# Performance work log

Hardware: AMD Instinct MI355X
Metric: run time of the kernel (lower is better)

The kernel has to match this reference:

```python
import jax, jax.numpy as jnp
import numpy as np

B = 262144
HIST = 24
FORE = 20
HID = 256
# torch: tau_int = clamp(tau,1,18).long().item(); default tau=6.0 -> static 6 (host sync in torch)
TAU_INT = 6


def setup_inputs() -> dict:
    key = jax.random.key(0)
    ks = jax.random.split(key, 9)
    s = 0.1
    return {
        "history": jax.random.normal(ks[0], (B, HIST), jnp.float32),
        "enc_w1": jax.random.normal(ks[1], (HIST + FORE, HID), jnp.float32) * s,
        "enc_b1": jnp.zeros((HID,), jnp.float32),
        "enc_w2": jax.random.normal(ks[2], (HID, HID), jnp.float32) * s,
        "enc_b2": jnp.zeros((HID,), jnp.float32),
        "cor_w1": jax.random.normal(ks[3], (HID, HID), jnp.float32) * s,
        "cor_b1": jnp.zeros((HID,), jnp.float32),
        "cor_w2": jax.random.normal(ks[4], (HID, FORE), jnp.float32) * s,
        "cor_b2": jnp.zeros((FORE,), jnp.float32),
        "alpha": jnp.float32(0.2),
        "beta": jnp.float32(0.3),
        "gamma": jnp.float32(0.01),
        "tau": jnp.float32(6.0),
        "lambda_mix": jnp.float32(0.5),
    }


def _physics_core(history, alpha, beta, gamma, steps):
    a = jax.nn.sigmoid(alpha)
    b = jax.nn.sigmoid(beta)
    g = jnp.abs(gamma)
    T0 = history[:, -1]                      # [B]
    buf0 = history[:, -TAU_INT:].T           # [tau, B]; buf0[0] = history[:, -tau]

    def step(carry, _):
        T, buf = carry
        T_delayed = buf[0]
        T_new = T - a * T - b * T_delayed - g * T ** 3
        buf = jnp.concatenate([buf[1:], T_new[None, :]], axis=0)
        return (T_new, buf), T_new

    _, preds = jax.lax.scan(step, (T0, buf0), None, length=steps)
    return preds.T                            # [B, steps]


def reference(history, enc_w1, enc_b1, enc_w2, enc_b2,
              cor_w1, cor_b1, cor_w2, cor_b2,
              alpha, beta, gamma, tau, lambda_mix):
    T_physics = _physics_core(history, alpha, beta, gamma, FORE)   # [B, FORE]
    combined = jnp.concatenate([history, T_physics], axis=1)       # [B, HIST+FORE]
    h = jnp.tanh(combined @ enc_w1 + enc_b1)
    features = jnp.tanh(h @ enc_w2 + enc_b2)
    c = jnp.tanh(features @ cor_w1 + cor_b1)
    T_soft = c @ cor_w2 + cor_b2                                   # [B, FORE]
    lam = jax.nn.sigmoid(lambda_mix)
    T_pred = T_physics + lam * T_soft
    return (T_pred, T_physics, T_soft)
```

## Files before the change

kernel.cpp:

```cpp
#include <hip/hip_runtime.h>
#include <hip/hip_bf16.h>

#define NROWS 262144
#define HISTC 24
#define FOREC 20

typedef __bf16        v8bf __attribute__((ext_vector_type(8)));
typedef float         v4f  __attribute__((ext_vector_type(4)));
typedef float         v2f  __attribute__((ext_vector_type(2)));
typedef unsigned int  v4u  __attribute__((ext_vector_type(4)));
typedef unsigned int  v2u  __attribute__((ext_vector_type(2)));

#define WS_WT1_OFF 64
#define WT1_ELEMS 16384
#define WT2_ELEMS 65536
#define WT3_ELEMS 65536
#define WT4R_ELEMS 65536

#define TANH_C 2.885390081777927f

__device__ __forceinline__ unsigned short f2bf(float x) {
    unsigned u = __builtin_bit_cast(unsigned, x);
    u += 0x7FFFu + ((u >> 16) & 1u);
    return (unsigned short)(u >> 16);
}

__device__ __forceinline__ unsigned packbf2(float a, float b) {
    unsigned ua = __builtin_bit_cast(unsigned, a) + 0x8000u;
    unsigned ub = __builtin_bit_cast(unsigned, b) + 0x8000u;
    return __builtin_amdgcn_perm(ub, ua, 0x07060302u);
}

__device__ __forceinline__ void lds_barrier() {
    asm volatile("s_waitcnt lgkmcnt(0)\n\ts_barrier" ::: "memory");
}

__global__ __launch_bounds__(256) void prep_kernel(
        const float* __restrict__ w1, const float* __restrict__ w2,
        const float* __restrict__ w3, const float* __restrict__ w4,
        const float* __restrict__ alpha, const float* __restrict__ beta,
        const float* __restrict__ gamma, const float* __restrict__ lmix,
        unsigned char* __restrict__ ws)
{
    __shared__ unsigned short tile[4][32 * 17];
    if (blockIdx.x == 104) {
        int t = threadIdx.x;
        float* wsf = (float*)ws;
        if (t == 0) wsf[0] = 1.0f / (1.0f + expf(-alpha[0]));
        else if (t == 1) wsf[1] = 1.0f / (1.0f + expf(-beta[0]));
        else if (t == 2) wsf[2] = fabsf(gamma[0]);
        else if (t == 3) wsf[3] = 1.0f / (1.0f + expf(-lmix[0]));
        return;
    }
    const int w    = threadIdx.x >> 6;
    const int lane = threadIdx.x & 63;
    const int g    = blockIdx.x * 4 + w;
    const float* src; int srcN, Kreal, Nreal, nt, kt;
    if (g < 32)       { src = w1; srcN = 256; Kreal = 44;  Nreal = 256; nt = g >> 1;  kt = g & 1; }
    else if (g < 160) { int t = g - 32;  src = w2; srcN = 256; Kreal = 256; Nreal = 256; nt = t >> 3; kt = t & 7; }
    else if (g < 288) { int t = g - 160; src = w3; srcN = 256; Kreal = 256; Nreal = 256; nt = t >> 3; kt = t & 7; }
    else              { int t = g - 288; src = w4; srcN = 20;  Kreal = 256; Nreal = 20;  nt = (t >> 3) & 1; kt = t & 7; }

    const int kbase = kt * 32;
    const int fl = lane & 15;
    const int rl = lane >> 4;
    const int feat = nt * 16 + fl;
    unsigned short* tl = tile[w];

#pragma unroll
    for (int it = 0; it < 8; ++it) {
        int row = it * 4 + rl;
        int k = kbase + row;
        float v = (k < Kreal && feat < Nreal) ? src[k * srcN + feat] : 0.0f;
        tl[row * 17 + fl] = f2bf(v);
    }
    __syncthreads();

    const int qq = lane >> 4;
    unsigned short e0 = tl[(qq * 8 + 0) * 17 + fl];
    unsigned short e1 = tl[(qq * 8 + 1) * 17 + fl];
    unsigned short e2 = tl[(qq * 8 + 2) * 17 + fl];
    unsigned short e3 = tl[(qq * 8 + 3) * 17 + fl];
    unsigned short e4 = tl[(qq * 8 + 4) * 17 + fl];
    unsigned short e5 = tl[(qq * 8 + 5) * 17 + fl];
    unsigned short e6 = tl[(qq * 8 + 6) * 17 + fl];
    unsigned short e7 = tl[(qq * 8 + 7) * 17 + fl];
    v4u pk;
    pk[0] = e0 | ((unsigned)e1 << 16);
    pk[1] = e2 | ((unsigned)e3 << 16);
    pk[2] = e4 | ((unsigned)e5 << 16);
    pk[3] = e6 | ((unsigned)e7 << 16);
    unsigned short* dst = (unsigned short*)(ws + WS_WT1_OFF);
    *(v4u*)&dst[(g * 64 + lane) * 8] = pk;
}

template<int KT, int KTN>
__device__ __forceinline__ void layer_pipe(unsigned short* buf,
        const v4u* __restrict__ wp, const v4u* __restrict__ wpn,
        const float* __restrict__ bias, v4u A[2][4],
        int w, int c, int q, int lane)
{
    v4f acc[4][4];
#pragma unroll
    for (int ft = 0; ft < 4; ++ft)
#pragma unroll
        for (int st = 0; st < 4; ++st) {
            v4f z = {0.0f, 0.0f, 0.0f, 0.0f};
            acc[ft][st] = z;
        }

#pragma unroll
    for (int kt = 0; kt < KT; ++kt) {
        const int cs = kt & 1;
        const int ps = cs ^ 1;
        if (kt + 1 < KT) {
#pragma unroll
            for (int ft = 0; ft < 4; ++ft)
                A[ps][ft] = wp[((w * 4 + ft) * KT + kt + 1) * 64 + lane];
        } else {
#pragma unroll
            for (int ft = 0; ft < 4; ++ft)
                A[ps][ft] = wpn[((w * 4 + ft) * KTN + 0) * 64 + lane];
        }
#pragma unroll
        for (int st = 0; st < 4; ++st) {
            v4u braw = *(const v4u*)&buf[(st * 16 + c) * 264 + kt * 32 + q * 8];
            v8bf bb = __builtin_bit_cast(v8bf, braw);
#pragma unroll
            for (int ft = 0; ft < 4; ++ft)
                acc[ft][st] = __builtin_amdgcn_mfma_f32_16x16x32_bf16(
                    __builtin_bit_cast(v8bf, A[cs][ft]), bb, acc[ft][st], 0, 0, 0);
        }
    }

    lds_barrier();

#pragma unroll
    for (int ft = 0; ft < 4; ++ft) {
        v4f bi = *(const v4f*)&bias[w * 64 + ft * 16 + q * 4];
        v4f bic;
#pragma unroll
        for (int r = 0; r < 4; ++r) bic[r] = bi[r] * TANH_C;
#pragma unroll
        for (int st = 0; st < 4; ++st) {
            float x[4];
#pragma unroll
            for (int r = 0; r < 4; ++r) {
                float t = __builtin_fmaf(acc[ft][st][r], TANH_C, bic[r]);
                float p = __builtin_amdgcn_exp2f(t);
                float rc = __builtin_amdgcn_rcpf(p + 1.0f);
                x[r] = __builtin_fmaf(-2.0f, rc, 1.0f);
            }
            v2u d; d[0] = packbf2(x[0], x[1]); d[1] = packbf2(x[2], x[3]);
            *(v2u*)&buf[(st * 16 + c) * 264 + w * 64 + ft * 16 + q * 4] = d;
        }
    }
    lds_barrier();
}

__global__ __launch_bounds__(256, 4) void fused_kernel(
    const float* __restrict__ history,
    const float* __restrict__ eb1, const float* __restrict__ eb2,
    const float* __restrict__ cb1, const float* __restrict__ cb2,
    const unsigned char* __restrict__ ws, float* __restrict__ out)
{
    __shared__ unsigned short buf[64 * 264];
    __shared__ float tp[64 * 20];

    const int tid  = threadIdx.x;
    const int w    = tid >> 6;
    const int lane = tid & 63;
    const int c    = lane & 15;
    const int q    = lane >> 4;
    const int row0 = blockIdx.x << 6;
    const float* wsf = (const float*)ws;
    const v4u* wp1 = (const v4u*)(ws + WS_WT1_OFF);
    const v4u* wp2 = wp1 + WT1_ELEMS / 8;
    const v4u* wp3 = wp2 + WT2_ELEMS / 8;
    const v4u* wp4 = wp3 + WT3_ELEMS / 8;

    v4u A[2][4];
#pragma unroll
    for (int ft = 0; ft < 4; ++ft)
        A[0][ft] = wp1[((w * 4 + ft) * 2 + 0) * 64 + lane];

#pragma unroll
    for (int i = 0; i < 2; ++i) {
        int e = tid + i * 256;
        if (e < 384) {
            int r  = e / 6, c4 = e - r * 6;
            v4f h4 = *(const v4f*)&history[(long)(row0 + r) * 24 + c4 * 4];
            v2u d; d[0] = packbf2(h4[0], h4[1]); d[1] = packbf2(h4[2], h4[3]);
            *(v2u*)&buf[r * 264 + c4 * 4] = d;
        }
    }
#pragma unroll
    for (int i = 0; i < 2; ++i) {
        int e = tid + i * 256;
        if (e < 320) {
            int r = e / 5, g = e - r * 5;
            v2u z = {0u, 0u};
            *(v2u*)&buf[r * 264 + 44 + g * 4] = z;
        }
    }
    if (tid < 64) {
        const float* hrow = &history[(long)(row0 + tid) * 24];
        v2f h18 = *(const v2f*)&hrow[18];
        v4f h20 = *(const v4f*)&hrow[20];
        float pa = wsf[0], pb = wsf[1], pg = wsf[2];
        float d0 = h18[0], d1 = h18[1], d2 = h20[0];
        float d3 = h20[1], d4 = h20[2], d5 = h20[3];
        float T = d5;
#pragma unroll
        for (int s = 0; s < 20; ++s) {
            float t3 = T * T * T;
            float Tn = T - pa * T;
            Tn = Tn - pb * d0;
            Tn = Tn - pg * t3;
            tp[tid * 20 + s] = Tn;
            buf[tid * 264 + 24 + s] = f2bf(Tn);
            d0 = d1; d1 = d2; d2 = d3; d3 = d4; d4 = d5; d5 = Tn;
            T = Tn;
        }
    }
    lds_barrier();

    layer_pipe<2, 8>(buf, wp1, wp2, eb1, A, w, c, q, lane);
    layer_pipe<8, 8>(buf, wp2, wp3, eb2, A, w, c, q, lane);
    layer_pipe<8, 8>(buf, wp3, wp4, cb1, A, w, c, q, lane);

    v4f acc40 = {0.0f, 0.0f, 0.0f, 0.0f}, acc41 = {0.0f, 0.0f, 0.0f, 0.0f};
#pragma unroll
    for (int kt = 0; kt < 8; ++kt) {
        const int cs = kt & 1, ps = cs ^ 1;
        if (kt + 1 < 8) {
            A[ps][0] = wp4[((w * 4 + 0) * 8 + kt + 1) * 64 + lane];
            A[ps][1] = wp4[((w * 4 + 1) * 8 + kt + 1) * 64 + lane];
        }
        v4u braw = *(const v4u*)&buf[(w * 16 + c) * 264 + kt * 32 + q * 8];
        v8bf bb = __builtin_bit_cast(v8bf, braw);
        acc40 = __builtin_amdgcn_mfma_f32_16x16x32_bf16(
            __builtin_bit_cast(v8bf, A[cs][0]), bb, acc40, 0, 0, 0);
        acc41 = __builtin_amdgcn_mfma_f32_16x16x32_bf16(
            __builtin_bit_cast(v8bf, A[cs][1]), bb, acc41, 0, 0, 0);
    }

    const float lam = wsf[3];
    const long sample = (long)row0 + w * 16 + c;
    float* outP = out;
    float* outF = out + (long)NROWS * 20;
    float* outS = out + (long)NROWS * 40;
    {
        int f0 = q * 4;
        v4f bi  = *(const v4f*)&cb2[f0];
        v4f tph = *(const v4f*)&tp[(w * 16 + c) * 20 + f0];
        v4f ts, pr;
#pragma unroll
        for (int r = 0; r < 4; ++r) {
            ts[r] = acc40[r] + bi[r];
            pr[r] = tph[r] + lam * ts[r];
        }
        *(v4f*)&outS[sample * 20 + f0] = ts;
        *(v4f*)&outP[sample * 20 + f0] = pr;
        *(v4f*)&outF[sample * 20 + f0] = tph;
    }
    if (q == 0) {
        v4f bi  = *(const v4f*)&cb2[16];
        v4f tph = *(const v4f*)&tp[(w * 16 + c) * 20 + 16];
        v4f ts, pr;
#pragma unroll
        for (int r = 0; r < 4; ++r) {
            ts[r] = acc41[r] + bi[r];
            pr[r] = tph[r] + lam * ts[r];
        }
        *(v4f*)&outS[sample * 20 + 16] = ts;
        *(v4f*)&outP[sample * 20 + 16] = pr;
        *(v4f*)&outF[sample * 20 + 16] = tph;
    }
}

extern "C" void kernel_launch(void* const* d_in, const int* in_sizes, int n_in,
                              void* d_out, int out_size, void* d_ws, size_t ws_size,
                              hipStream_t stream)
{
    const float* history = (const float*)d_in[0];
    const float* enc_w1  = (const float*)d_in[1];
    const float* enc_b1  = (const float*)d_in[2];
    const float* enc_w2  = (const float*)d_in[3];
    const float* enc_b2  = (const float*)d_in[4];
    const float* cor_w1  = (const float*)d_in[5];
    const float* cor_b1  = (const float*)d_in[6];
    const float* cor_w2  = (const float*)d_in[7];
    const float* cor_b2  = (const float*)d_in[8];
    const float* alpha   = (const float*)d_in[9];
    const float* beta    = (const float*)d_in[10];
    const float* gamma   = (const float*)d_in[11];
    const float* lmix    = (const float*)d_in[13];

    prep_kernel<<<105, 256, 0, stream>>>(enc_w1, enc_w2, cor_w1, cor_w2,
                                         alpha, beta, gamma, lmix,
                                         (unsigned char*)d_ws);
    fused_kernel<<<NROWS / 64, 256, 0, stream>>>(history, enc_b1, enc_b2, cor_b1, cor_b2,
                                                 (const unsigned char*)d_ws, (float*)d_out);
}
```

Measured before the change: 208.2 us.

## Double-buffer activations in XOR-swizzled LDS and recompute physics in registers

Activations now ping-pong between two 64x256 bf16 LDS buffers instead of one padded buffer. This removes the barrier that separated the MFMA reads from the tanh writeback in each layer. The LDS layout moves from row padding of 264 to an XOR swizzle on 8-element groups, to avoid bank conflicts without the padding. The fp32 physics trajectory is no longer kept in LDS; each lane recomputes it in registers from history before writing outputs, trading extra ALU work and a global reload of history for less LDS use. Total LDS grows from about 38.9 KB to 64 KB per block, which may limit how many blocks fit per CU.

```diff
diff --git a/kernel.cpp b/kernel.cpp
--- a/kernel.cpp
+++ b/kernel.cpp
@@ -33,6 +33,10 @@
 
 __device__ __forceinline__ void lds_barrier() {
     asm volatile("s_waitcnt lgkmcnt(0)\n\ts_barrier" ::: "memory");
+}
+
+__device__ __forceinline__ int swz(int row, int col) {
+    return row * 256 + ((((col >> 3) ^ (row & 7)) << 3) | (col & 7));
 }
 
 __global__ __launch_bounds__(256) void prep_kernel(
@@ -95,7 +99,8 @@
 }
 
 template<int KT, int KTN>
-__device__ __forceinline__ void layer_pipe(unsigned short* buf,
+__device__ __forceinline__ void layer_pipe(
+        const unsigned short* __restrict__ bin, unsigned short* __restrict__ bout,
         const v4u* __restrict__ wp, const v4u* __restrict__ wpn,
         const float* __restrict__ bias, v4u A[2][4],
         int w, int c, int q, int lane)
@@ -124,7 +129,7 @@
         }
 #pragma unroll
         for (int st = 0; st < 4; ++st) {
-            v4u braw = *(const v4u*)&buf[(st * 16 + c) * 264 + kt * 32 + q * 8];
+            v4u braw = *(const v4u*)&bin[swz(st * 16 + c, kt * 32 + q * 8)];
             v8bf bb = __builtin_bit_cast(v8bf, braw);
 #pragma unroll
             for (int ft = 0; ft < 4; ++ft)
@@ -132,8 +137,6 @@
                     __builtin_bit_cast(v8bf, A[cs][ft]), bb, acc[ft][st], 0, 0, 0);
         }
     }
-
-    lds_barrier();
 
 #pragma unroll
     for (int ft = 0; ft < 4; ++ft) {
@@ -152,7 +155,7 @@
                 x[r] = __builtin_fmaf(-2.0f, rc, 1.0f);
             }
             v2u d; d[0] = packbf2(x[0], x[1]); d[1] = packbf2(x[2], x[3]);
-            *(v2u*)&buf[(st * 16 + c) * 264 + w * 64 + ft * 16 + q * 4] = d;
+            *(v2u*)&bout[swz(st * 16 + c, w * 64 + ft * 16 + q * 4)] = d;
         }
     }
     lds_barrier();
@@ -164,8 +167,8 @@
     const float* __restrict__ cb1, const float* __restrict__ cb2,
     const unsigned char* __restrict__ ws, float* __restrict__ out)
 {
-    __shared__ unsigned short buf[64 * 264];
-    __shared__ float tp[64 * 20];
+    __shared__ unsigned short bufA[64 * 256];
+    __shared__ unsigned short bufB[64 * 256];
 
     const int tid  = threadIdx.x;
     const int w    = tid >> 6;
@@ -191,7 +194,7 @@
             int r  = e / 6, c4 = e - r * 6;
             v4f h4 = *(const v4f*)&history[(long)(row0 + r) * 24 + c4 * 4];
             v2u d; d[0] = packbf2(h4[0], h4[1]); d[1] = packbf2(h4[2], h4[3]);
-            *(v2u*)&buf[r * 264 + c4 * 4] = d;
+            *(v2u*)&bufA[swz(r, c4 * 4)] = d;
         }
     }
 #pragma unroll
@@ -200,7 +203,7 @@
         if (e < 320) {
             int r = e / 5, g = e - r * 5;
             v2u z = {0u, 0u};
-            *(v2u*)&buf[r * 264 + 44 + g * 4] = z;
+            *(v2u*)&bufA[swz(r, 44 + g * 4)] = z;
         }
     }
     if (tid < 64) {
@@ -217,17 +220,16 @@
             float Tn = T - pa * T;
             Tn = Tn - pb * d0;
             Tn = Tn - pg * t3;
-            tp[tid * 20 + s] = Tn;
-            buf[tid * 264 + 24 + s] = f2bf(Tn);
+            bufA[swz(tid, 24 + s)] = f2bf(Tn);
             d0 = d1; d1 = d2; d2 = d3; d3 = d4; d4 = d5; d5 = Tn;
             T = Tn;
         }
     }
     lds_barrier();
 
-    layer_pipe<2, 8>(buf, wp1, wp2, eb1, A, w, c, q, lane);
-    layer_pipe<8, 8>(buf, wp2, wp3, eb2, A, w, c, q, lane);
-    layer_pipe<8, 8>(buf, wp3, wp4, cb1, A, w, c, q, lane);
+    layer_pipe<2, 8>(bufA, bufB, wp1, wp2, eb1, A, w, c, q, lane);
+    layer_pipe<8, 8>(bufB, bufA, wp2, wp3, eb2, A, w, c, q, lane);
+    layer_pipe<8, 8>(bufA, bufB, wp3, wp4, cb1, A, w, c, q, lane);
 
     v4f acc40 = {0.0f, 0.0f, 0.0f, 0.0f}, acc41 = {0.0f, 0.0f, 0.0f, 0.0f};
 #pragma unroll
@@ -237,7 +239,7 @@
             A[ps][0] = wp4[((w * 4 + 0) * 8 + kt + 1) * 64 + lane];
             A[ps][1] = wp4[((w * 4 + 1) * 8 + kt + 1) * 64 + lane];
         }
-        v4u braw = *(const v4u*)&buf[(w * 16 + c) * 264 + kt * 32 + q * 8];
+        v4u braw = *(const v4u*)&bufB[swz(w * 16 + c, kt * 32 + q * 8)];
         v8bf bb = __builtin_bit_cast(v8bf, braw);
         acc40 = __builtin_amdgcn_mfma_f32_16x16x32_bf16(
             __builtin_bit_cast(v8bf, A[cs][0]), bb, acc40, 0, 0, 0);
@@ -245,15 +247,38 @@
             __builtin_bit_cast(v8bf, A[cs][1]), bb, acc41, 0, 0, 0);
     }
 
+    const long sample = (long)row0 + w * 16 + c;
+    float Tv[20];
+    {
+        const float* hrow = &history[sample * 24];
+        v2f h18 = *(const v2f*)&hrow[18];
+        v4f h20 = *(const v4f*)&hrow[20];
+        float pa = wsf[0], pb = wsf[1], pg = wsf[2];
+        float d0 = h18[0], d1 = h18[1], d2 = h20[0];
+        float d3 = h20[1], d4 = h20[2], d5 = h20[3];
+        float T = d5;
+#pragma unroll
+        for (int s = 0; s < 20; ++s) {
+            float t3 = T * T * T;
+            float Tn = T - pa * T;
+            Tn = Tn - pb * d0;
+            Tn = Tn - pg * t3;
+            Tv[s] = Tn;
+            d0 = d1; d1 = d2; d2 = d3; d3 = d4; d4 = d5; d5 = Tn;
+            T = Tn;
+        }
+    }
     const float lam = wsf[3];
-    const long sample = (long)row0 + w * 16 + c;
     float* outP = out;
     float* outF = out + (long)NROWS * 20;
     float* outS = out + (long)NROWS * 40;
     {
         int f0 = q * 4;
         v4f bi  = *(const v4f*)&cb2[f0];
-        v4f tph = *(const v4f*)&tp[(w * 16 + c) * 20 + f0];
+        v4f tph;
+#pragma unroll
+        for (int r = 0; r < 4; ++r)
+            tph[r] = q == 0 ? Tv[0 + r] : q == 1 ? Tv[4 + r] : q == 2 ? Tv[8 + r] : Tv[12 + r];
         v4f ts, pr;
 #pragma unroll
         for (int r = 0; r < 4; ++r) {
@@ -266,7 +291,7 @@
     }
     if (q == 0) {
         v4f bi  = *(const v4f*)&cb2[16];
-        v4f tph = *(const v4f*)&tp[(w * 16 + c) * 20 + 16];
+        v4f tph; tph[0] = Tv[16]; tph[1] = Tv[17]; tph[2] = Tv[18]; tph[3] = Tv[19];
         v4f ts, pr;
 #pragma unroll
         for (int r = 0; r < 4; ++r) {
```

Measured after the change: 217.2 us. 4.3% more time.
